# Optimization experiments

Measured on AMD Instinct MI355X. Metric: run time of the kernel, lower is better.

The kernel has to match this reference:

```python
import jax, jax.numpy as jnp
import numpy as np

B, H, W, C = 8, 28, 28, 1024
NH = 16
HD = C // NH          # head dim 64
HID = 4 * C           # mlp hidden 4096
BC = C // 2           # bottleneck channels 512
SCALE = HD ** -0.5


def setup_inputs() -> dict:
    key = jax.random.key(0)
    ks = iter(jax.random.split(key, 32))
    def rn(shape, s=0.02):
        return jax.random.normal(next(ks), shape, jnp.float32) * s
    return dict(
        x=jax.random.normal(next(ks), (B, H, W, C), jnp.float32),
        norm1_w=jnp.ones((C,), jnp.float32), norm1_b=jnp.zeros((C,), jnp.float32),
        qkv_w=rn((C, 3 * C)), qkv_b=jnp.zeros((3 * C,), jnp.float32),
        proj_w=rn((C, C)), proj_b=jnp.zeros((C,), jnp.float32),
        rel_h=rn((2 * H - 1, HD)), rel_w=rn((2 * W - 1, HD)),
        norm2_w=jnp.ones((C,), jnp.float32), norm2_b=jnp.zeros((C,), jnp.float32),
        fc1_w=rn((C, HID)), fc1_b=jnp.zeros((HID,), jnp.float32),
        fc2_w=rn((HID, C)), fc2_b=jnp.zeros((C,), jnp.float32),
        conv1_w=rn((1, 1, C, BC)), ln1_w=jnp.ones((BC,), jnp.float32), ln1_b=jnp.zeros((BC,), jnp.float32),
        conv2_w=rn((3, 3, BC, BC)), ln2_w=jnp.ones((BC,), jnp.float32), ln2_b=jnp.zeros((BC,), jnp.float32),
        conv3_w=rn((1, 1, BC, C)), ln3_w=rn((C,)), ln3_b=rn((C,)),
    )


def _ln(x, w, b, eps):
    # layernorm over last axis (channels in NHWC)
    m = jnp.mean(x, -1, keepdims=True)
    v = jnp.mean((x - m) ** 2, -1, keepdims=True)
    return (x - m) * jax.lax.rsqrt(v + eps) * w + b


def _conv(x, w, pad):
    return jax.lax.conv_general_dilated(
        x, w, (1, 1), pad, dimension_numbers=('NHWC', 'HWIO', 'NHWC'))


def _gelu(x):
    return jax.nn.gelu(x, approximate=False)


def _block_forward(x, norm1_w, norm1_b, qkv_w, qkv_b, proj_w, proj_b,
                   rel_h, rel_w, norm2_w, norm2_b, fc1_w, fc1_b, fc2_w, fc2_b,
                   conv1_w, ln1_w, ln1_b, conv2_w, ln2_w, ln2_b, conv3_w, ln3_w, ln3_b):
    S = H * W
    shortcut = x
    xn = _ln(x, norm1_w, norm1_b, 1e-5)

    # ---- attention with decomposed relative position bias ----
    qkv = xn.reshape(B, S, C) @ qkv_w + qkv_b                 # [B,S,3C]
    qkv = qkv.reshape(B, S, 3, NH, HD).transpose(2, 0, 3, 1, 4)  # [3,B,nh,S,hd]
    q, k, v = qkv[0], qkv[1], qkv[2]
    attn = jnp.einsum('bnsd,bntd->bnst', q * SCALE, k)        # [B,nh,S,S]

    idx_h = jnp.arange(H)[:, None] - jnp.arange(H)[None, :] + (H - 1)
    idx_w = jnp.arange(W)[:, None] - jnp.arange(W)[None, :] + (W - 1)
    Rh = rel_h[idx_h]   # [H,H,hd]
    Rw = rel_w[idx_w]   # [W,W,hd]
    qr = q.reshape(B, NH, H, W, HD)
    bias_h = jnp.einsum('bnhwd,hkd->bnhwk', qr, Rh)           # [B,nh,H,W,H]
    bias_w = jnp.einsum('bnhwd,wkd->bnhwk', qr, Rw)           # [B,nh,H,W,W]
    attn = (attn.reshape(B, NH, H, W, H, W)
            + bias_h[..., :, None] + bias_w[..., None, :]).reshape(B, NH, S, S)

    attn = jax.nn.softmax(attn, axis=-1)
    out = jnp.einsum('bnst,bntd->bnsd', attn, v)              # [B,nh,S,hd]
    out = out.transpose(0, 2, 1, 3).reshape(B, H, W, C)
    out = out @ proj_w + proj_b

    x = shortcut + out

    # ---- MLP ----
    xn = _ln(x, norm2_w, norm2_b, 1e-5)
    x = x + (_gelu(xn.reshape(B, S, C) @ fc1_w + fc1_b) @ fc2_w + fc2_b).reshape(B, H, W, C)

    # ---- residual bottleneck conv (channel LayerNorm, eps=1e-6) ----
    out = _conv(x, conv1_w, 'VALID')
    out = _gelu(_ln(out, ln1_w, ln1_b, 1e-6))
    out = _conv(out, conv2_w, ((1, 1), (1, 1)))
    out = _gelu(_ln(out, ln2_w, ln2_b, 1e-6))
    out = _conv(out, conv3_w, 'VALID')
    out = _ln(out, ln3_w, ln3_b, 1e-6)
    return x + out


def reference(x, norm1_w, norm1_b, qkv_w, qkv_b, proj_w, proj_b,
              rel_h, rel_w, norm2_w, norm2_b, fc1_w, fc1_b, fc2_w, fc2_b,
              conv1_w, ln1_w, ln1_b, conv2_w, ln2_w, ln2_b, conv3_w, ln3_w, ln3_b):
    return _block_forward(x, norm1_w, norm1_b, qkv_w, qkv_b, proj_w, proj_b,
                          rel_h, rel_w, norm2_w, norm2_b, fc1_w, fc1_b, fc2_w, fc2_b,
                          conv1_w, ln1_w, ln1_b, conv2_w, ln2_w, ln2_b, conv3_w, ln3_w, ln3_b)
```

## Files before the change

kernel.cpp:

```cpp
#include <hip/hip_runtime.h>
#include <cstdint>
#include <cstddef>

using u16 = unsigned short;
using u32 = unsigned int;

__device__ __forceinline__ float bf2f(u16 u){
  union { u32 i; float f; } x; x.i = ((u32)u) << 16; return x.f;
}
__device__ __forceinline__ u16 f2bf(float f){
  union { float f; u32 i; } x; x.f = f;
  u32 r = x.i + 0x7fffu + ((x.i >> 16) & 1u);
  return (u16)(r >> 16);
}
__device__ __forceinline__ float gelu_f(float x){
  return 0.5f * x * (1.0f + erff(x * 0.70710678118654752f));
}
__device__ __forceinline__ void gld16(const void* g, void* l){
  __builtin_amdgcn_global_load_lds((__attribute__((address_space(1))) void*)(void*)g,
                                   (__attribute__((address_space(3))) void*)l, 16, 0, 0);
}

typedef __bf16 bf16x8 __attribute__((ext_vector_type(8)));
typedef float  f32x4  __attribute__((ext_vector_type(4)));
typedef u16    u16x4  __attribute__((ext_vector_type(4)));

__global__ __launch_bounds__(256) void k_transpose(const float* __restrict__ src,
                                                   u16* __restrict__ dst, int R, int C){
  __shared__ u16 tile[32][33];
  int bx = blockIdx.x * 32;
  int by = blockIdx.y * 32;
  int tx = threadIdx.x & 31;
  int ty = threadIdx.x >> 5;
  for (int r = ty; r < 32; r += 8)
    tile[r][tx] = f2bf(src[(size_t)(by + r) * C + bx + tx]);
  __syncthreads();
  for (int r = ty; r < 32; r += 8)
    dst[(size_t)(bx + r) * R + by + tx] = tile[tx][r];
}

template<bool IN_F32, bool DO_GELU>
__global__ __launch_bounds__(256) void k_layernorm(const void* __restrict__ inp,
    const float* __restrict__ w, const float* __restrict__ bsh,
    u16* __restrict__ out, int cols, float eps){
  int row = blockIdx.x, t = threadIdx.x;
  size_t base = (size_t)row * cols;
  const float* inf = (const float*)inp;
  const u16*  inb = (const u16*)inp;
  float v[4];
  int ep = cols >> 8;
  float s = 0.f, ss = 0.f;
  for (int e = 0; e < ep; ++e){
    int idx = t + (e << 8);
    float x = IN_F32 ? inf[base + idx] : bf2f(inb[base + idx]);
    v[e] = x; s += x; ss += x * x;
  }
#pragma unroll
  for (int off = 1; off < 64; off <<= 1){
    s  += __shfl_xor(s, off, 64);
    ss += __shfl_xor(ss, off, 64);
  }
  __shared__ float red[8];
  int wv = t >> 6;
  if ((t & 63) == 0){ red[wv] = s; red[4 + wv] = ss; }
  __syncthreads();
  s  = red[0] + red[1] + red[2] + red[3];
  ss = red[4] + red[5] + red[6] + red[7];
  float inv = 1.f / (float)cols;
  float mean = s * inv;
  float var = ss * inv - mean * mean;
  float rs = rsqrtf(var + eps);
  for (int e = 0; e < ep; ++e){
    int idx = t + (e << 8);
    float y = (v[e] - mean) * rs * w[idx] + bsh[idx];
    if (DO_GELU) y = gelu_f(y);
    out[base + idx] = f2bf(y);
  }
}

__global__ __launch_bounds__(256) void k_final(const u16* __restrict__ c3,
    const u16* __restrict__ x2, const float* __restrict__ w,
    const float* __restrict__ bsh, float* __restrict__ out){
  int row = blockIdx.x, t = threadIdx.x;
  size_t base = (size_t)row << 10;
  float v[4];
  float s = 0.f, ss = 0.f;
#pragma unroll
  for (int e = 0; e < 4; ++e){
    int idx = t + (e << 8);
    float x = bf2f(c3[base + idx]);
    v[e] = x; s += x; ss += x * x;
  }
#pragma unroll
  for (int off = 1; off < 64; off <<= 1){
    s  += __shfl_xor(s, off, 64);
    ss += __shfl_xor(ss, off, 64);
  }
  __shared__ float red[8];
  int wv = t >> 6;
  if ((t & 63) == 0){ red[wv] = s; red[4 + wv] = ss; }
  __syncthreads();
  s  = red[0] + red[1] + red[2] + red[3];
  ss = red[4] + red[5] + red[6] + red[7];
  float mean = s * (1.f/1024.f);
  float var = ss * (1.f/1024.f) - mean * mean;
  float rs = rsqrtf(var + 1e-6f);
#pragma unroll
  for (int e = 0; e < 4; ++e){
    int idx = t + (e << 8);
    float y = (v[e] - mean) * rs * w[idx] + bsh[idx];
    out[base + idx] = bf2f(x2[base + idx]) + y;
  }
}

template<bool BIAS, bool GELU, bool RES, bool OUTB, bool OUTF>
__global__ __launch_bounds__(256, 2) void k_gemm(
    const u16* __restrict__ A, const u16* __restrict__ Bt,
    const float* __restrict__ bias, const float* __restrict__ resf,
    u16* __restrict__ outb, float* __restrict__ outf, int N, int K)
{
  __shared__ __align__(16) u16 As[128 * 32];
  __shared__ __align__(16) u16 Bs[128 * 32];
  int t = threadIdx.x, lane = t & 63, wv = t >> 6;
  int m0 = blockIdx.y << 7, n0 = blockIdx.x << 7;
  int wm = (wv >> 1) << 6, wn = (wv & 1) << 6;

  f32x4 acc[4][4];
  const f32x4 z4 = {0.f, 0.f, 0.f, 0.f};
#pragma unroll
  for (int i = 0; i < 4; ++i)
#pragma unroll
    for (int j = 0; j < 4; ++j) acc[i][j] = z4;

  int srow = (wv << 5) + (lane >> 2);
  int skp  = (lane & 3) << 3;
  const u16* Ag = A  + (size_t)(m0 + srow) * K + skp;
  const u16* Bg = Bt + (size_t)(n0 + srow) * K + skp;
  u16* As0 = &As[(wv << 5) * 32];
  u16* As1 = As0 + 16 * 32;
  u16* Bs0 = &Bs[(wv << 5) * 32];
  u16* Bs1 = Bs0 + 16 * 32;
  const size_t rowskip = (size_t)16 * K;

  int fr = lane & 15, fq = (lane >> 4) << 3;

  for (int k0 = 0; k0 < K; k0 += 32){
    gld16(Ag + k0, As0);
    gld16(Ag + rowskip + k0, As1);
    gld16(Bg + k0, Bs0);
    gld16(Bg + rowskip + k0, Bs1);
    __syncthreads();
    bf16x8 af[4], bfr[4];
#pragma unroll
    for (int i = 0; i < 4; ++i)
      af[i] = *(const bf16x8*)&As[(wm + i * 16 + fr) * 32 + fq];
#pragma unroll
    for (int j = 0; j < 4; ++j)
      bfr[j] = *(const bf16x8*)&Bs[(wn + j * 16 + fr) * 32 + fq];
#pragma unroll
    for (int i = 0; i < 4; ++i)
#pragma unroll
      for (int j = 0; j < 4; ++j)
        acc[i][j] = __builtin_amdgcn_mfma_f32_16x16x32_bf16(af[i], bfr[j], acc[i][j], 0, 0, 0);
    __syncthreads();
  }

  int rr = (lane >> 4) << 2;
  int cc = lane & 15;
#pragma unroll
  for (int i = 0; i < 4; ++i)
#pragma unroll
    for (int j = 0; j < 4; ++j){
      int gc = n0 + wn + j * 16 + cc;
      float bb = BIAS ? bias[gc] : 0.f;
#pragma unroll
      for (int r = 0; r < 4; ++r){
        int gr = m0 + wm + i * 16 + rr + r;
        size_t idx = (size_t)gr * N + gc;
        float vv = acc[i][j][r] + bb;
        if (RES) vv += resf[idx];
        if (GELU) vv = gelu_f(vv);
        if (OUTF) outf[idx] = vv;
        if (OUTB) outb[idx] = f2bf(vv);
      }
    }
}

__global__ __launch_bounds__(256) void k_vtrans(const u16* __restrict__ qkv, u16* __restrict__ vtg){
  __shared__ u32 tile[64][33];
  int bnh = blockIdx.x;
  int st  = blockIdx.y;
  int b = bnh >> 4, nh = bnh & 15;
  int t = threadIdx.x;
  int tx = t & 31;
  int ty = t >> 5;
  const u16* src = qkv + (size_t)b * 784 * 3072 + 2048 + nh * 64;
  int s0 = st << 6;
  for (int r = ty; r < 64; r += 8){
    int s = s0 + r;
    u32 val = 0u;
    if (s < 784) val = *(const u32*)(src + (size_t)s * 3072 + tx * 2);
    tile[r][tx] = val;
  }
  __syncthreads();
  u16* dst = vtg + (size_t)bnh * 64 * 832 + s0;
  for (int d = ty; d < 64; d += 8){
    u32 lo = tile[2 * tx][d >> 1];
    u32 hi = tile[2 * tx + 1][d >> 1];
    u16 a  = (d & 1) ? (u16)(lo >> 16) : (u16)lo;
    u16 bb = (d & 1) ? (u16)(hi >> 16) : (u16)hi;
    u32 pk = (u32)a | ((u32)bb << 16);
    *(u32*)(dst + (size_t)d * 832 + 2 * tx) = pk;
  }
}

#define ATT_STR 72
#define GSTR 132
#define LOG2E 1.4426950408889634f
__global__ __launch_bounds__(256, 3) void k_attn5(const u16* __restrict__ qkv,
    const float* __restrict__ relh, const float* __restrict__ relw,
    const u16* __restrict__ vtg, u16* __restrict__ out)
{
  __shared__ __align__(16) u16 p_s[128 * ATT_STR];
  __shared__ __align__(16) u16 gh_t[28 * GSTR];
  __shared__ __align__(16) u16 gw_t[28 * GSTR];

  const int t = threadIdx.x, lane = t & 63, wv = t >> 6;
  int id = blockIdx.x;
  int xr = id & 7, rest = id >> 3;
  int qt = rest % 7, gg = rest / 7;
  int bnh = xr + (gg << 3);
  const int b = bnh >> 4, nh = bnh & 15;
  const int q0 = qt << 7;
  const size_t rowbase = (size_t)b * 784;
  const int wq0 = wv << 5;
  const int fr = lane & 15;
  const int fq = lane >> 4;

  u16* rh_s = p_s;
  u16* rw_s = p_s + 64 * ATT_STR;
  {
    int row = t >> 2, c0 = (t & 3) << 4;
    u16 bh_[16], bw_[16];
    if (row < 55){
      const float* ph = relh + row * 64 + c0;
      const float* pw = relw + row * 64 + c0;
#pragma unroll
      for (int e = 0; e < 16; ++e){ bh_[e] = f2bf(ph[e]); bw_[e] = f2bf(pw[e]); }
    } else {
#pragma unroll
      for (int e = 0; e < 16; ++e){ bh_[e] = 0; bw_[e] = 0; }
    }
    *(uint4*)&rh_s[row * ATT_STR + c0]     = *(uint4*)bh_;
    *(uint4*)&rh_s[row * ATT_STR + c0 + 8] = *(uint4*)(bh_ + 8);
    *(uint4*)&rw_s[row * ATT_STR + c0]     = *(uint4*)bw_;
    *(uint4*)&rw_s[row * ATT_STR + c0 + 8] = *(uint4*)(bw_ + 8);
  }

  bf16x8 qf[2][2];
#pragma unroll
  for (int mf = 0; mf < 2; ++mf)
#pragma unroll
    for (int ks = 0; ks < 2; ++ks){
      int row = q0 + wq0 + mf * 16 + fr;
      if (row < 784){
        qf[mf][ks] = *(const bf16x8*)(qkv + (rowbase + row) * 3072 + nh * 64 + fq * 8 + ks * 32);
      } else {
        uint4 z = {0u,0u,0u,0u}; qf[mf][ks] = *(bf16x8*)&z;
      }
    }
  __syncthreads();

  const f32x4 z4 = {0.f,0.f,0.f,0.f};
#pragma unroll
  for (int which = 0; which < 2; ++which){
    const u16* rs = which ? rw_s : rh_s;
    f32x4 G[2][4];
#pragma unroll
    for (int mf = 0; mf < 2; ++mf)
#pragma unroll
      for (int nf = 0; nf < 4; ++nf) G[mf][nf] = z4;
#pragma unroll
    for (int nf = 0; nf < 4; ++nf){
      bf16x8 rf0 = *(const bf16x8*)&rs[(nf * 16 + fr) * ATT_STR + fq * 8];
      bf16x8 rf1 = *(const bf16x8*)&rs[(nf * 16 + fr) * ATT_STR + fq * 8 + 32];
#pragma unroll
      for (int mf = 0; mf < 2; ++mf){
        G[mf][nf] = __builtin_amdgcn_mfma_f32_16x16x32_bf16(qf[mf][0], rf0, G[mf][nf], 0, 0, 0);
        G[mf][nf] = __builtin_amdgcn_mfma_f32_16x16x32_bf16(qf[mf][1], rf1, G[mf][nf], 0, 0, 0);
      }
    }
    u16* gt = which ? gw_t : gh_t;
#pragma unroll
    for (int mf = 0; mf < 2; ++mf)
#pragma unroll
      for (int r = 0; r < 4; ++r){
        int lr = wq0 + mf * 16 + fq * 4 + r;
        int grow = q0 + lr;
        int hq = grow / 28;
        int coord = which ? (grow - hq * 28) : hq;
#pragma unroll
        for (int nf = 0; nf < 4; ++nf){
          int j = nf * 16 + fr;
          int kk = coord + 27 - j;
          if ((unsigned)kk < 28u) gt[kk * GSTR + lr] = f2bf(G[mf][nf][r] * LOG2E);
        }
      }
  }
  __syncthreads();

  f32x4 acc[2][5];
#pragma unroll
  for (int mf = 0; mf < 2; ++mf)
#pragma unroll
    for (int nf = 0; nf < 5; ++nf) acc[mf][nf] = z4;

  u16 onesu[8];
#pragma unroll
  for (int e = 0; e < 8; ++e) onesu[e] = 0x3f80;
  bf16x8 onesf = *(bf16x8*)onesu;

  const u16* kgb = qkv + rowbase * 3072 + 1024 + nh * 64 + fq * 8;
  const u16* vgb = vtg + ((size_t)bnh * 64 + fr) * 832 + fq * 8;

  bf16x8 kf[4][2];
  {
#pragma unroll
    for (int nf = 0; nf < 4; ++nf){
      int jg = nf * 16 + fr;
      const u16* kp = kgb + (size_t)jg * 3072;
      kf[nf][0] = *(const bf16x8*)kp;
      kf[nf][1] = *(const bf16x8*)(kp + 32);
    }
  }

  const float SSC = 0.125f * LOG2E;

  for (int kt = 0; kt < 13; ++kt){
    const int ktb = kt << 6;

    bf16x8 vf[2][4];
#pragma unroll
    for (int ks = 0; ks < 2; ++ks)
#pragma unroll
      for (int nf = 0; nf < 4; ++nf)
        vf[ks][nf] = *(const bf16x8*)(vgb + (size_t)(nf * 16) * 832 + ktb + ks * 32);

    f32x4 S[2][4];
#pragma unroll
    for (int nf = 0; nf < 4; ++nf){
#pragma unroll
      for (int mf = 0; mf < 2; ++mf){
        f32x4 s = z4;
        s = __builtin_amdgcn_mfma_f32_16x16x32_bf16(qf[mf][0], kf[nf][0], s, 0, 0, 0);
        s = __builtin_amdgcn_mfma_f32_16x16x32_bf16(qf[mf][1], kf[nf][1], s, 0, 0, 0);
        S[mf][nf] = s;
      }
    }

    {
      int ktn = (kt < 12 ? kt + 1 : 12) << 6;
#pragma unroll
      for (int nf = 0; nf < 4; ++nf){
        int jg = ktn + nf * 16 + fr;
        int jc = jg < 784 ? jg : 783;
        const u16* kp = kgb + (size_t)jc * 3072;
        kf[nf][0] = *(const bf16x8*)kp;
        kf[nf][1] = *(const bf16x8*)(kp + 32);
      }
    }

    int hj[4], wj[4]; bool val[4];
#pragma unroll
    for (int nf = 0; nf < 4; ++nf){
      int jg = ktb + nf * 16 + fr;
      int h = jg / 28;
      hj[nf] = h; wj[nf] = jg - h * 28; val[nf] = (jg < 784);
    }

#pragma unroll
    for (int mf = 0; mf < 2; ++mf){
      int lrb = wq0 + mf * 16 + fq * 4;
#pragma unroll
      for (int nf = 0; nf < 4; ++nf){
        u16x4 h4 = *(const u16x4*)&gh_t[hj[nf] * GSTR + lrb];
        u16x4 w4 = *(const u16x4*)&gw_t[wj[nf] * GSTR + lrb];
#pragma unroll
        for (int r = 0; r < 4; ++r){
          float p = 0.f;
          if (val[nf])
            p = exp2f(fmaf(SSC, S[mf][nf][r], bf2f(h4[r]) + bf2f(w4[r])));
          p_s[(lrb + r) * ATT_STR + nf * 16 + fr] = f2bf(p);
        }
      }
    }

#pragma unroll
    for (int ks = 0; ks < 2; ++ks){
      bf16x8 pf0 = *(const bf16x8*)&p_s[(wq0 + fr) * ATT_STR + fq * 8 + ks * 32];
      bf16x8 pf1 = *(const bf16x8*)&p_s[(wq0 + 16 + fr) * ATT_STR + fq * 8 + ks * 32];
#pragma unroll
      for (int nf = 0; nf < 4; ++nf){
        acc[0][nf] = __builtin_amdgcn_mfma_f32_16x16x32_bf16(pf0, vf[ks][nf], acc[0][nf], 0, 0, 0);
        acc[1][nf] = __builtin_amdgcn_mfma_f32_16x16x32_bf16(pf1, vf[ks][nf], acc[1][nf], 0, 0, 0);
      }
      acc[0][4] = __builtin_amdgcn_mfma_f32_16x16x32_bf16(pf0, onesf, acc[0][4], 0, 0, 0);
      acc[1][4] = __builtin_amdgcn_mfma_f32_16x16x32_bf16(pf1, onesf, acc[1][4], 0, 0, 0);
    }
  }

#pragma unroll
  for (int mf = 0; mf < 2; ++mf)
#pragma unroll
    for (int r = 0; r < 4; ++r){
      int row = q0 + wq0 + mf * 16 + fq * 4 + r;
      if (row < 784){
        float inv = 1.f / acc[mf][4][r];
        u16* dp = out + (rowbase + row) * 1024 + nh * 64 + fr;
#pragma unroll
        for (int nf = 0; nf < 4; ++nf)
          dp[nf * 16] = f2bf(acc[mf][nf][r] * inv);
      }
    }
}

__global__ __launch_bounds__(256) void k_im2col(const u16* __restrict__ g, u16* __restrict__ im){
  int idx = blockIdx.x * 256 + threadIdx.x;
  int p  = idx / 576;
  int c8 = idx - p * 576;
  int k0 = c8 << 3;
  int t9 = k0 >> 9;
  int ci = k0 & 511;
  int ky = t9 / 3, kx = t9 - ky * 3;
  int bb = p / 784;
  int s = p - bb * 784;
  int h = s / 28, w = s - h * 28;
  int hh = h + ky - 1, ww = w + kx - 1;
  uint4 val = make_uint4(0u, 0u, 0u, 0u);
  if ((unsigned)hh < 28u && (unsigned)ww < 28u)
    val = *(const uint4*)&g[(((size_t)(bb * 28 + hh)) * 28 + ww) * 512 + ci];
  *(uint4*)&im[(size_t)p * 4608 + k0] = val;
}

extern "C" void kernel_launch(void* const* d_in, const int* in_sizes, int n_in,
                              void* d_out, int out_size, void* d_ws, size_t ws_size,
                              hipStream_t stream)
{
  (void)in_sizes; (void)n_in; (void)out_size; (void)ws_size;
  const float* x      = (const float*)d_in[0];
  const float* n1w    = (const float*)d_in[1];
  const float* n1b    = (const float*)d_in[2];
  const float* qkv_w  = (const float*)d_in[3];
  const float* qkv_b  = (const float*)d_in[4];
  const float* proj_w = (const float*)d_in[5];
  const float* proj_b = (const float*)d_in[6];
  const float* rel_h  = (const float*)d_in[7];
  const float* rel_w  = (const float*)d_in[8];
  const float* n2w    = (const float*)d_in[9];
  const float* n2b    = (const float*)d_in[10];
  const float* fc1_w  = (const float*)d_in[11];
  const float* fc1_b  = (const float*)d_in[12];
  const float* fc2_w  = (const float*)d_in[13];
  const float* fc2_b  = (const float*)d_in[14];
  const float* c1w    = (const float*)d_in[15];
  const float* l1w    = (const float*)d_in[16];
  const float* l1b    = (const float*)d_in[17];
  const float* c2w    = (const float*)d_in[18];
  const float* l2w    = (const float*)d_in[19];
  const float* l2b    = (const float*)d_in[20];
  const float* c3w    = (const float*)d_in[21];
  const float* l3w    = (const float*)d_in[22];
  const float* l3b    = (const float*)d_in[23];

  char* ws = (char*)d_ws;
  size_t off = 0;
  auto alloc = [&](size_t bytes) -> void* {
    void* p = ws + off; off += (bytes + 255) & ~(size_t)255; return p;
  };
  const size_t M = 6272;
  u16* qkvT  = (u16*)alloc((size_t)3072 * 1024 * 2);
  u16* projT = (u16*)alloc((size_t)1024 * 1024 * 2);
  u16* fc1T  = (u16*)alloc((size_t)4096 * 1024 * 2);
  u16* fc2T  = (u16*)alloc((size_t)1024 * 4096 * 2);
  u16* c1T   = (u16*)alloc((size_t)512 * 1024 * 2);
  u16* c2T   = (u16*)alloc((size_t)512 * 4608 * 2);
  u16* c3T   = (u16*)alloc((size_t)1024 * 512 * 2);
  u16* qkvbuf = (u16*)alloc(M * 3072 * 2);
  u16* attn   = (u16*)alloc(M * 1024 * 2);
  u16* xn     = (u16*)alloc(M * 1024 * 2);
  float* x1   = (float*)alloc(M * 1024 * 4);
  u16* x2b    = (u16*)alloc(M * 1024 * 2);
  u16* c1buf  = (u16*)alloc(M * 512 * 2);
  u16* g1buf  = (u16*)alloc(M * 512 * 2);
  u16* hmlp   = qkvbuf;
  u16* im     = qkvbuf;
  u16* xn2    = xn;
  u16* c2buf  = c1buf;
  u16* g2buf  = g1buf;
  u16* c3buf  = attn;
  u16* vtg    = (u16*)x1;

  dim3 blk(256);
  k_transpose<<<dim3(3072/32, 1024/32), blk, 0, stream>>>(qkv_w, qkvT, 1024, 3072);
  k_transpose<<<dim3(1024/32, 1024/32), blk, 0, stream>>>(proj_w, projT, 1024, 1024);
  k_transpose<<<dim3(4096/32, 1024/32), blk, 0, stream>>>(fc1_w, fc1T, 1024, 4096);
  k_transpose<<<dim3(1024/32, 4096/32), blk, 0, stream>>>(fc2_w, fc2T, 4096, 1024);
  k_transpose<<<dim3(512/32, 1024/32),  blk, 0, stream>>>(c1w, c1T, 1024, 512);
  k_transpose<<<dim3(512/32, 4608/32),  blk, 0, stream>>>(c2w, c2T, 4608, 512);
  k_transpose<<<dim3(1024/32, 512/32),  blk, 0, stream>>>(c3w, c3T, 512, 1024);

  k_layernorm<true,false><<<6272, blk, 0, stream>>>(x, n1w, n1b, xn, 1024, 1e-5f);
  k_gemm<true,false,false,true,false><<<dim3(24,49), blk, 0, stream>>>(
      xn, qkvT, qkv_b, nullptr, qkvbuf, nullptr, 3072, 1024);
  k_vtrans<<<dim3(128, 13), blk, 0, stream>>>(qkvbuf, vtg);
  k_attn5<<<896, blk, 0, stream>>>(qkvbuf, rel_h, rel_w, vtg, attn);
  k_gemm<true,false,true,false,true><<<dim3(8,49), blk, 0, stream>>>(
      attn, projT, proj_b, x, nullptr, x1, 1024, 1024);
  k_layernorm<true,false><<<6272, blk, 0, stream>>>(x1, n2w, n2b, xn2, 1024, 1e-5f);
  k_gemm<true,true,false,true,false><<<dim3(32,49), blk, 0, stream>>>(
      xn2, fc1T, fc1_b, nullptr, hmlp, nullptr, 4096, 1024);
  k_gemm<true,false,true,true,false><<<dim3(8,49), blk, 0, stream>>>(
      hmlp, fc2T, fc2_b, x1, x2b, nullptr, 1024, 4096);
  k_gemm<false,false,false,true,false><<<dim3(4,49), blk, 0, stream>>>(
      x2b, c1T, nullptr, nullptr, c1buf, nullptr, 512, 1024);
  k_layernorm<false,true><<<6272, blk, 0, stream>>>(c1buf, l1w, l1b, g1buf, 512, 1e-6f);
  k_im2col<<<14112, blk, 0, stream>>>(g1buf, im);
  k_gemm<false,false,false,true,false><<<dim3(4,49), blk, 0, stream>>>(
      im, c2T, nullptr, nullptr, c2buf, nullptr, 512, 4608);
  k_layernorm<false,true><<<6272, blk, 0, stream>>>(c2buf, l2w, l2b, g2buf, 512, 1e-6f);
  k_gemm<false,false,false,true,false><<<dim3(8,49), blk, 0, stream>>>(
      g2buf, c3T, nullptr, nullptr, c3buf, nullptr, 1024, 512);
  k_final<<<6272, blk, 0, stream>>>(c3buf, x2b, l3w, l3b, (float*)d_out);
}
```

Baseline: 761.1 us.

## Use single-wave attention blocks and XCD-aware GEMM tile remapping

The attention kernel drops from 256-thread blocks covering 128 queries to 64-thread single-wave blocks covering 32 queries. This removes the __syncthreads barriers, shrinks shared memory, and raises the block count to 3200. Relative-position tables are now read from global memory and converted in registers instead of being staged in shared memory. K fragments are loaded per iteration instead of prefetched, which may expose load latency. The GEMM block index is also remapped so that consecutive tiles land on the same XCD, to improve L2 locality.

Measured after the change: 761.4 us. Within noise of the previous version (+0.1%).

```diff
diff --git a/kernel.cpp b/kernel.cpp
--- a/kernel.cpp
+++ b/kernel.cpp
@@ -122,7 +122,17 @@
   __shared__ __align__(16) u16 As[128 * 32];
   __shared__ __align__(16) u16 Bs[128 * 32];
   int t = threadIdx.x, lane = t & 63, wv = t >> 6;
-  int m0 = blockIdx.y << 7, n0 = blockIdx.x << 7;
+
+  int nbx = gridDim.x;
+  int nwg = nbx * gridDim.y;
+  int li  = blockIdx.y * nbx + blockIdx.x;
+  int qc = nwg >> 3, rc = nwg & 7;
+  int xcd = li & 7, jj = li >> 3;
+  int wg = (xcd < rc ? xcd * (qc + 1) : rc * (qc + 1) + (xcd - rc) * qc) + jj;
+  int byy = wg / nbx;
+  int bxx = wg - byy * nbx;
+  int m0 = byy << 7, n0 = bxx << 7;
+
   int wm = (wv >> 1) << 6, wn = (wv & 1) << 6;
 
   f32x4 acc[4][4];
@@ -214,67 +224,46 @@
   }
 }
 
-#define ATT_STR 72
-#define GSTR 132
+#define PST 72
+#define GT  36
 #define LOG2E 1.4426950408889634f
-__global__ __launch_bounds__(256, 3) void k_attn5(const u16* __restrict__ qkv,
+__global__ __launch_bounds__(64, 3) void k_attn6(const u16* __restrict__ qkv,
     const float* __restrict__ relh, const float* __restrict__ relw,
     const u16* __restrict__ vtg, u16* __restrict__ out)
 {
-  __shared__ __align__(16) u16 p_s[128 * ATT_STR];
-  __shared__ __align__(16) u16 gh_t[28 * GSTR];
-  __shared__ __align__(16) u16 gw_t[28 * GSTR];
-
-  const int t = threadIdx.x, lane = t & 63, wv = t >> 6;
-  int id = blockIdx.x;
-  int xr = id & 7, rest = id >> 3;
-  int qt = rest % 7, gg = rest / 7;
-  int bnh = xr + (gg << 3);
+  __shared__ __align__(16) u16 p_s[32 * PST];
+  __shared__ __align__(16) u16 gh_t[28 * GT];
+  __shared__ __align__(16) u16 gw_t[28 * GT];
+
+  const int lane = threadIdx.x & 63;
+  int i = blockIdx.x;
+  int o = (i & 7) * 400 + (i >> 3);
+  int bnh = o / 25;
+  int rem = o - bnh * 25;
   const int b = bnh >> 4, nh = bnh & 15;
-  const int q0 = qt << 7;
+  const int q0 = rem << 5;
   const size_t rowbase = (size_t)b * 784;
-  const int wq0 = wv << 5;
   const int fr = lane & 15;
   const int fq = lane >> 4;
 
-  u16* rh_s = p_s;
-  u16* rw_s = p_s + 64 * ATT_STR;
-  {
-    int row = t >> 2, c0 = (t & 3) << 4;
-    u16 bh_[16], bw_[16];
-    if (row < 55){
-      const float* ph = relh + row * 64 + c0;
-      const float* pw = relw + row * 64 + c0;
-#pragma unroll
-      for (int e = 0; e < 16; ++e){ bh_[e] = f2bf(ph[e]); bw_[e] = f2bf(pw[e]); }
-    } else {
-#pragma unroll
-      for (int e = 0; e < 16; ++e){ bh_[e] = 0; bw_[e] = 0; }
-    }
-    *(uint4*)&rh_s[row * ATT_STR + c0]     = *(uint4*)bh_;
-    *(uint4*)&rh_s[row * ATT_STR + c0 + 8] = *(uint4*)(bh_ + 8);
-    *(uint4*)&rw_s[row * ATT_STR + c0]     = *(uint4*)bw_;
-    *(uint4*)&rw_s[row * ATT_STR + c0 + 8] = *(uint4*)(bw_ + 8);
-  }
-
   bf16x8 qf[2][2];
 #pragma unroll
   for (int mf = 0; mf < 2; ++mf)
 #pragma unroll
     for (int ks = 0; ks < 2; ++ks){
-      int row = q0 + wq0 + mf * 16 + fr;
+      int row = q0 + mf * 16 + fr;
       if (row < 784){
         qf[mf][ks] = *(const bf16x8*)(qkv + (rowbase + row) * 3072 + nh * 64 + fq * 8 + ks * 32);
       } else {
         uint4 z = {0u,0u,0u,0u}; qf[mf][ks] = *(bf16x8*)&z;
       }
     }
-  __syncthreads();
 
   const f32x4 z4 = {0.f,0.f,0.f,0.f};
+
 #pragma unroll
   for (int which = 0; which < 2; ++which){
-    const u16* rs = which ? rw_s : rh_s;
+    const float* R = which ? relw : relh;
     f32x4 G[2][4];
 #pragma unroll
     for (int mf = 0; mf < 2; ++mf)
@@ -282,8 +271,19 @@
       for (int nf = 0; nf < 4; ++nf) G[mf][nf] = z4;
 #pragma unroll
     for (int nf = 0; nf < 4; ++nf){
-      bf16x8 rf0 = *(const bf16x8*)&rs[(nf * 16 + fr) * ATT_STR + fq * 8];
-      bf16x8 rf1 = *(const bf16x8*)&rs[(nf * 16 + fr) * ATT_STR + fq * 8 + 32];
+      int row = nf * 16 + fr;
+      bf16x8 rf0, rf1;
+      if (row < 55){
+        const float* p = R + row * 64 + fq * 8;
+        u16 tmp[16];
+#pragma unroll
+        for (int e = 0; e < 8; ++e) tmp[e]     = f2bf(p[e]);
+#pragma unroll
+        for (int e = 0; e < 8; ++e) tmp[8 + e] = f2bf(p[32 + e]);
+        rf0 = *(bf16x8*)tmp; rf1 = *(bf16x8*)(tmp + 8);
+      } else {
+        uint4 z = {0u,0u,0u,0u}; rf0 = *(bf16x8*)&z; rf1 = rf0;
+      }
 #pragma unroll
       for (int mf = 0; mf < 2; ++mf){
         G[mf][nf] = __builtin_amdgcn_mfma_f32_16x16x32_bf16(qf[mf][0], rf0, G[mf][nf], 0, 0, 0);
@@ -295,7 +295,7 @@
     for (int mf = 0; mf < 2; ++mf)
 #pragma unroll
       for (int r = 0; r < 4; ++r){
-        int lr = wq0 + mf * 16 + fq * 4 + r;
+        int lr = mf * 16 + fq * 4 + r;
         int grow = q0 + lr;
         int hq = grow / 28;
         int coord = which ? (grow - hq * 28) : hq;
@@ -303,11 +303,10 @@
         for (int nf = 0; nf < 4; ++nf){
           int j = nf * 16 + fr;
           int kk = coord + 27 - j;
-          if ((unsigned)kk < 28u) gt[kk * GSTR + lr] = f2bf(G[mf][nf][r] * LOG2E);
+          if ((unsigned)kk < 28u) gt[kk * GT + lr] = f2bf(G[mf][nf][r] * LOG2E);
         }
       }
   }
-  __syncthreads();
 
   f32x4 acc[2][5];
 #pragma unroll
@@ -323,82 +322,61 @@
   const u16* kgb = qkv + rowbase * 3072 + 1024 + nh * 64 + fq * 8;
   const u16* vgb = vtg + ((size_t)bnh * 64 + fr) * 832 + fq * 8;
 
-  bf16x8 kf[4][2];
-  {
+  const float SSC = 0.125f * LOG2E;
+
+  for (int kt = 0; kt < 13; ++kt){
+    const int ktb = kt << 6;
+
+    bf16x8 vf[2][4];
+#pragma unroll
+    for (int ks = 0; ks < 2; ++ks)
+#pragma unroll
+      for (int nf = 0; nf < 4; ++nf)
+        vf[ks][nf] = *(const bf16x8*)(vgb + (size_t)(nf * 16) * 832 + ktb + ks * 32);
+
+    bf16x8 kf[4][2];
 #pragma unroll
     for (int nf = 0; nf < 4; ++nf){
-      int jg = nf * 16 + fr;
-      const u16* kp = kgb + (size_t)jg * 3072;
+      int jg = ktb + nf * 16 + fr;
+      int jc = jg < 784 ? jg : 783;
+      const u16* kp = kgb + (size_t)jc * 3072;
       kf[nf][0] = *(const bf16x8*)kp;
       kf[nf][1] = *(const bf16x8*)(kp + 32);
     }
-  }
-
-  const float SSC = 0.125f * LOG2E;
-
-  for (int kt = 0; kt < 13; ++kt){
-    const int ktb = kt << 6;
-
-    bf16x8 vf[2][4];
-#pragma unroll
-    for (int ks = 0; ks < 2; ++ks)
-#pragma unroll
-      for (int nf = 0; nf < 4; ++nf)
-        vf[ks][nf] = *(const bf16x8*)(vgb + (size_t)(nf * 16) * 832 + ktb + ks * 32);
-
-    f32x4 S[2][4];
+
 #pragma unroll
     for (int nf = 0; nf < 4; ++nf){
+      f32x4 S[2];
 #pragma unroll
       for (int mf = 0; mf < 2; ++mf){
         f32x4 s = z4;
         s = __builtin_amdgcn_mfma_f32_16x16x32_bf16(qf[mf][0], kf[nf][0], s, 0, 0, 0);
         s = __builtin_amdgcn_mfma_f32_16x16x32_bf16(qf[mf][1], kf[nf][1], s, 0, 0, 0);
-        S[mf][nf] = s;
-      }
-    }
-
-    {
-      int ktn = (kt < 12 ? kt + 1 : 12) << 6;
-#pragma unroll
-      for (int nf = 0; nf < 4; ++nf){
-        int jg = ktn + nf * 16 + fr;
-        int jc = jg < 784 ? jg : 783;
-        const u16* kp = kgb + (size_t)jc * 3072;
-        kf[nf][0] = *(const bf16x8*)kp;
-        kf[nf][1] = *(const bf16x8*)(kp + 32);
-      }
-    }
-
-    int hj[4], wj[4]; bool val[4];
-#pragma unroll
-    for (int nf = 0; nf < 4; ++nf){
+        S[mf] = s;
+      }
       int jg = ktb + nf * 16 + fr;
       int h = jg / 28;
-      hj[nf] = h; wj[nf] = jg - h * 28; val[nf] = (jg < 784);
-    }
-
-#pragma unroll
-    for (int mf = 0; mf < 2; ++mf){
-      int lrb = wq0 + mf * 16 + fq * 4;
-#pragma unroll
-      for (int nf = 0; nf < 4; ++nf){
-        u16x4 h4 = *(const u16x4*)&gh_t[hj[nf] * GSTR + lrb];
-        u16x4 w4 = *(const u16x4*)&gw_t[wj[nf] * GSTR + lrb];
+      int w = jg - h * 28;
+      bool val = (jg < 784);
+#pragma unroll
+      for (int mf = 0; mf < 2; ++mf){
+        int lrb = mf * 16 + fq * 4;
+        u16x4 h4 = *(const u16x4*)&gh_t[h * GT + lrb];
+        u16x4 w4 = *(const u16x4*)&gw_t[w * GT + lrb];
 #pragma unroll
         for (int r = 0; r < 4; ++r){
           float p = 0.f;
-          if (val[nf])
-            p = exp2f(fmaf(SSC, S[mf][nf][r], bf2f(h4[r]) + bf2f(w4[r])));
-          p_s[(lrb + r) * ATT_STR + nf * 16 + fr] = f2bf(p);
+          if (val)
+            p = exp2f(fmaf(SSC, S[mf][r], bf2f(h4[r]) + bf2f(w4[r])));
+          p_s[(lrb + r) * PST + nf * 16 + fr] = f2bf(p);
         }
       }
     }
 
 #pragma unroll
     for (int ks = 0; ks < 2; ++ks){
-      bf16x8 pf0 = *(const bf16x8*)&p_s[(wq0 + fr) * ATT_STR + fq * 8 + ks * 32];
-      bf16x8 pf1 = *(const bf16x8*)&p_s[(wq0 + 16 + fr) * ATT_STR + fq * 8 + ks * 32];
+      bf16x8 pf0 = *(const bf16x8*)&p_s[(fr) * PST + fq * 8 + ks * 32];
+      bf16x8 pf1 = *(const bf16x8*)&p_s[(16 + fr) * PST + fq * 8 + ks * 32];
 #pragma unroll
       for (int nf = 0; nf < 4; ++nf){
         acc[0][nf] = __builtin_amdgcn_mfma_f32_16x16x32_bf16(pf0, vf[ks][nf], acc[0][nf], 0, 0, 0);
@@ -413,7 +391,7 @@
   for (int mf = 0; mf < 2; ++mf)
 #pragma unroll
     for (int r = 0; r < 4; ++r){
-      int row = q0 + wq0 + mf * 16 + fq * 4 + r;
+      int row = q0 + mf * 16 + fq * 4 + r;
       if (row < 784){
         float inv = 1.f / acc[mf][4][r];
         u16* dp = out + (rowbase + row) * 1024 + nh * 64 + fr;
@@ -513,7 +491,7 @@
   k_gemm<true,false,false,true,false><<<dim3(24,49), blk, 0, stream>>>(
       xn, qkvT, qkv_b, nullptr, qkvbuf, nullptr, 3072, 1024);
   k_vtrans<<<dim3(128, 13), blk, 0, stream>>>(qkvbuf, vtg);
-  k_attn5<<<896, blk, 0, stream>>>(qkvbuf, rel_h, rel_w, vtg, attn);
+  k_attn6<<<3200, dim3(64), 0, stream>>>(qkvbuf, rel_h, rel_w, vtg, attn);
   k_gemm<true,false,true,false,true><<<dim3(8,49), blk, 0, stream>>>(
       attn, projT, proj_b, x, nullptr, x1, 1024, 1024);
   k_layernorm<true,false><<<6272, blk, 0, stream>>>(x1, n2w, n2b, xn2, 1024, 1e-5f);
```
